# Kernel tuning notes

Hardware: AMD Instinct MI355X
Metric: run time of the kernel (lower is better)

## Reference

```python
import jax, jax.numpy as jnp
import numpy as np

C = 32
C_Z = 128
S = 256
N_SEQ = 256
LN_EPS = 1e-5


def setup_inputs() -> dict:
    key = jax.random.key(0)
    k1, k2, k3, k4 = jax.random.split(key, 4)
    m_si = jax.random.normal(k1, (S, N_SEQ, C), dtype=jnp.float32)
    ln_gamma = jnp.ones((C,), dtype=jnp.float32)
    ln_beta = jnp.zeros((C,), dtype=jnp.float32)
    # nn.Linear(c, 2c, bias=False): weight shape (2c, c)
    W_ab = jax.random.normal(k2, (2 * C, C), dtype=jnp.float32) / np.sqrt(C)
    # nn.Linear(c*c, c_z): weight (c_z, c*c), bias (c_z,)
    W_out = jax.random.normal(k3, (C_Z, C * C), dtype=jnp.float32) / np.sqrt(C * C)
    b_out = jax.random.normal(k4, (C_Z,), dtype=jnp.float32) * 0.01
    return {"m_si": m_si, "ln_gamma": ln_gamma, "ln_beta": ln_beta,
            "W_ab": W_ab, "W_out": W_out, "b_out": b_out}


def reference(m_si, ln_gamma, ln_beta, W_ab, W_out, b_out):
    # LayerNorm over channel dim c
    mu = jnp.mean(m_si, axis=-1, keepdims=True)
    var = jnp.var(m_si, axis=-1, keepdims=True)
    x = (m_si - mu) * jax.lax.rsqrt(var + LN_EPS) * ln_gamma + ln_beta
    # linear_no_bias then chunk into a, b: each (s, n_seq, c)
    ab = jnp.einsum('snc,dc->snd', x, W_ab)
    a, b = ab[..., :C], ab[..., C:]
    # mean over MSA sequences of outer products a[s,i,:] x b[s,j,:]
    # restructured as a contraction over n_seq: (i, j, c, c)
    outer = jnp.einsum('inc,jnd->ijcd', a, b) / N_SEQ
    outer = outer.reshape(S, S, C * C)  # flatten (c, c) -> c*c
    # final linear projection to c_z
    z_ij = jnp.einsum('ijk,zk->ijz', outer, W_out) + b_out
    return z_ij
```

## Files before the change

kernel.cpp:

```cpp
#include <hip/hip_runtime.h>

#define SDIM 256
#define NSEQ 256
#define CDIM 32
#define CZ 128
#define IB 8
#define JB 4

typedef __bf16 bfx8 __attribute__((ext_vector_type(8)));
typedef float fx4 __attribute__((ext_vector_type(4)));
typedef float f32x16 __attribute__((ext_vector_type(16)));
typedef unsigned int u32x4 __attribute__((ext_vector_type(4)));

__device__ __forceinline__ unsigned short f2bf(float f) {
  unsigned int u = __float_as_uint(f);
  u += 0x7fffu + ((u >> 16) & 1u);
  return (unsigned short)(u >> 16);
}

__device__ __forceinline__ unsigned int cvtpk(float lo, float hi) {
  unsigned int r;
  asm("v_cvt_pk_bf16_f32 %0, %1, %2" : "=v"(r) : "v"(lo), "v"(hi));
  return r;
}

__device__ __forceinline__ bfx8 pack8(const fx4 lo, const fx4 hi) {
  bfx8 r;
  r[0] = (__bf16)lo[0]; r[1] = (__bf16)lo[1]; r[2] = (__bf16)lo[2]; r[3] = (__bf16)lo[3];
  r[4] = (__bf16)hi[0]; r[5] = (__bf16)hi[1]; r[6] = (__bf16)hi[2]; r[7] = (__bf16)hi[3];
  return r;
}

__device__ __forceinline__ void gload16(const void* g, void* l) {
  __builtin_amdgcn_global_load_lds((const __attribute__((address_space(1))) unsigned int*)g,
                                   (__attribute__((address_space(3))) unsigned int*)l,
                                   16, 0, 0);
}


__global__ __launch_bounds__(256) void opm_prep(
    const float* __restrict__ m_si, const float* __restrict__ gamma, const float* __restrict__ beta,
    const float* __restrict__ Wab, const float* __restrict__ Wout,
    unsigned short* __restrict__ a_t, unsigned short* __restrict__ b_t,
    unsigned short* __restrict__ w2T)
{
  __shared__ __align__(16) char shbuf[8192];
  const int b = blockIdx.x;
  const int t = threadIdx.x;
  if (b < SDIM) {
    const int s = b;
    const int l = t & 63;
    const int w = t >> 6;
    const int nl = l & 15;
    const int cg = l >> 4;

    bfx8 afr[4];
#pragma unroll
    for (int dt = 0; dt < 4; ++dt) {
      const float* wr = Wab + (dt * 16 + nl) * 32 + cg * 8;
      afr[dt] = pack8(*(const fx4*)wr, *(const fx4*)(wr + 4));
    }
    const fx4 g0 = *(const fx4*)(gamma + cg * 8);
    const fx4 g1 = *(const fx4*)(gamma + cg * 8 + 4);
    const fx4 bt0 = *(const fx4*)(beta + cg * 8);
    const fx4 bt1 = *(const fx4*)(beta + cg * 8 + 4);

#pragma unroll
    for (int p = 0; p < 4; ++p) {
      const int n = p * 64 + w * 16 + nl;
      const float* xr = m_si + (s * 256 + n) * 32 + cg * 8;
      const fx4 v0 = *(const fx4*)xr;
      const fx4 v1 = *(const fx4*)(xr + 4);
      float ps  = v0[0] + v0[1] + v0[2] + v0[3] + v1[0] + v1[1] + v1[2] + v1[3];
      float ps2 = v0[0]*v0[0] + v0[1]*v0[1] + v0[2]*v0[2] + v0[3]*v0[3]
                + v1[0]*v1[0] + v1[1]*v1[1] + v1[2]*v1[2] + v1[3]*v1[3];
      ps  += __shfl_xor(ps, 16);  ps  += __shfl_xor(ps, 32);
      ps2 += __shfl_xor(ps2, 16); ps2 += __shfl_xor(ps2, 32);
      const float mu = ps * 0.03125f;
      const float var = ps2 * 0.03125f - mu * mu;
      const float inv = rsqrtf(var + 1e-5f);
      const fx4 e0 = (v0 - mu) * inv * g0 + bt0;
      const fx4 e1 = (v1 - mu) * inv * g1 + bt1;
      const bfx8 bfr = pack8(e0, e1);

      fx4 dz[4];
#pragma unroll
      for (int dt = 0; dt < 4; ++dt)
        dz[dt] = __builtin_amdgcn_mfma_f32_16x16x32_bf16(afr[dt], bfr, (fx4){0.f,0.f,0.f,0.f}, 0, 0, 0);

#pragma unroll
      for (int dt = 0; dt < 4; ++dt) {
#pragma unroll
        for (int r = 0; r < 4; ++r) {
          const int d = dt * 16 + cg * 4 + r;
          const unsigned short hv = f2bf(dz[dt][r]);
          if (d < 32) a_t[(s * 32 + d) * 256 + n] = hv;
          else        b_t[(s * 32 + (d - 32)) * 256 + n] = hv;
        }
      }
    }
  } else {
    unsigned short* lin = (unsigned short*)shbuf;
    const int blk = b - SDIM;
    const float* wsrc = Wout + blk * 4096;
#pragma unroll
    for (int jj = 0; jj < 4; ++jj) {
      const int q = t + jj * 256;
      const fx4 v = ((const fx4*)wsrc)[q];
      unsigned short* dst = lin + q * 4;
      dst[0] = f2bf(v[0]); dst[1] = f2bf(v[1]); dst[2] = f2bf(v[2]); dst[3] = f2bf(v[3]);
    }
    __syncthreads();
    const int z0 = blk * 4;
#pragma unroll
    for (int w = 0; w < 2; ++w) {
      const int id = t + w * 256;
      const int lz = id & 3;
      const int hh = (id >> 2) & 1;
      const int ks = id >> 3;
      const int z = z0 + lz;
      unsigned short vals[8];
#pragma unroll
      for (int e = 0; e < 8; ++e) {
        const int kp = ks * 16 + hh * 8 + e;
        const int c = (kp & 3) | (((kp >> 8) & 1) << 2) | (((kp >> 2) & 1) << 3) | (((kp >> 9) & 1) << 4);
        const int d = (kp >> 3) & 31;
        vals[e] = lin[lz * 1024 + c * CDIM + d];
      }
      const int dest = ((z >> 5) << 15) + (ks << 9) + (hh << 8) + ((z & 31) << 3);
      *(u32x4*)(w2T + dest) = *(const u32x4*)vals;
    }
  }
}

__global__ __launch_bounds__(512, 4) void opm_main(
    const unsigned short* __restrict__ a_t, const unsigned short* __restrict__ b_t,
    const unsigned short* __restrict__ w2T, const float* __restrict__ bout,
    float* __restrict__ out)
{
  __shared__ __align__(16) char smem[65536];
  char* o_sh = smem;

  const int tid = threadIdx.x;
  const int lane = tid & 63;
  const int wid = tid >> 6;
  const int l31 = lane & 31;
  const int h = lane >> 5;

  const int bxr = blockIdx.x;
  const int xc = bxr & 7;
  const int q8 = bxr >> 3;
  const int it = q8 >> 4;
  const int jt = q8 & 15;
  const int i0 = ((xc & 1) * 16 + it) * IB;
  const int j0 = ((xc >> 1) * 16 + jt) * JB;

  const int wm = wid >> 1;
  const int wn = wid & 1;
  const int wbase = wid * 1024;

  f32x16 acc00 = {}, acc01 = {}, acc10 = {}, acc11 = {};

  auto STAGE = [&](int buf, int nc) {
    const int nbase = nc * 32;
    char* A = smem + 16384 + buf * 16384;
    char* B = smem + 49152 + buf * 8192;
#pragma unroll
    for (int pass = 0; pass < 2; ++pass) {
      const int q = pass * 512 + tid;
      const int row = q >> 2;
      const int gs = (q & 3) ^ ((q >> 3) & 3);
      const unsigned short* src = a_t + ((i0 + (row >> 5)) * 32 + (row & 31)) * 256 + nbase + gs * 8;
      gload16(src, A + pass * 8192 + wbase);
    }
    {
      const int q = tid;
      const int row = q >> 2;
      const int gs = (q & 3) ^ ((q >> 3) & 3);
      const unsigned short* src = b_t + ((j0 + (row >> 5)) * 32 + (row & 31)) * 256 + nbase + gs * 8;
      gload16(src, B + wbase);
    }
  };

  auto COMPUTE = [&](int buf) {
    char* A = smem + 16384 + buf * 16384;
    char* B = smem + 49152 + buf * 8192;
#pragma unroll
    for (int ks = 0; ks < 2; ++ks) {
      const int s = ks * 2 + h;
      bfx8 af0, af1, bf0, bf1;
      { const int r = wm * 64 + l31;      af0 = *(const bfx8*)(A + r * 64 + (((s ^ (r >> 1)) & 3) << 4)); }
      { const int r = wm * 64 + 32 + l31; af1 = *(const bfx8*)(A + r * 64 + (((s ^ (r >> 1)) & 3) << 4)); }
      { const int r = wn * 64 + l31;      bf0 = *(const bfx8*)(B + r * 64 + (((s ^ (r >> 1)) & 3) << 4)); }
      { const int r = wn * 64 + 32 + l31; bf1 = *(const bfx8*)(B + r * 64 + (((s ^ (r >> 1)) & 3) << 4)); }
      __builtin_amdgcn_s_setprio(1);
      acc00 = __builtin_amdgcn_mfma_f32_32x32x16_bf16(af0, bf0, acc00, 0, 0, 0);
      acc01 = __builtin_amdgcn_mfma_f32_32x32x16_bf16(af0, bf1, acc01, 0, 0, 0);
      acc10 = __builtin_amdgcn_mfma_f32_32x32x16_bf16(af1, bf0, acc10, 0, 0, 0);
      acc11 = __builtin_amdgcn_mfma_f32_32x32x16_bf16(af1, bf1, acc11, 0, 0, 0);
      __builtin_amdgcn_s_setprio(0);
    }
  };

  STAGE(0, 0);
#pragma unroll 2
  for (int t = 0; t < 8; ++t) {
    if (t < 7) {
      STAGE((t + 1) & 1, t + 1);
      asm volatile("s_waitcnt vmcnt(3)" ::: "memory");
    } else {
      asm volatile("s_waitcnt vmcnt(0)" ::: "memory");
    }
    __builtin_amdgcn_s_barrier();
    asm volatile("" ::: "memory");
    COMPUTE(t & 1);
    asm volatile("s_waitcnt lgkmcnt(0)" ::: "memory");
    __builtin_amdgcn_s_barrier();
  }

  {
    const f32x16 av[4] = { acc00 * 0.00390625f, acc01 * 0.00390625f,
                           acc10 * 0.00390625f, acc11 * 0.00390625f };
#pragma unroll
    for (int mi = 0; mi < 2; ++mi) {
#pragma unroll
      for (int ni = 0; ni < 2; ++ni) {
        const f32x16 a = av[mi * 2 + ni];
        const int p = (wm * 2 + mi) * 4 + (wn * 2 + ni);
#pragma unroll
        for (int c4 = 0; c4 < 2; ++c4) {
          const int sl = l31 + 32 * h + 64 * c4;
          u32x4 v;
          v[0] = cvtpk(a[8 * c4 + 0], a[8 * c4 + 1]);
          v[1] = cvtpk(a[8 * c4 + 2], a[8 * c4 + 3]);
          v[2] = cvtpk(a[8 * c4 + 4], a[8 * c4 + 5]);
          v[3] = cvtpk(a[8 * c4 + 6], a[8 * c4 + 7]);
          *(u32x4*)(o_sh + p * 2048 + ((sl ^ (p & 7)) << 4)) = v;
        }
      }
    }
  }
  __syncthreads();

  {
    const int ztp = wid & 1;
    const int kh = wid >> 1;
    const unsigned short* wpa = w2T + ((ztp * 2 + 0) << 15) + (h << 8) + (l31 << 3);
    const unsigned short* wpb = w2T + ((ztp * 2 + 1) << 15) + (h << 8) + (l31 << 3);
    const int obase = l31 * 2048;
    const int oxor = l31 & 7;
    const int ks0 = kh * 16;

    bfx8 wa[4], wb[4];
#pragma unroll
    for (int q = 0; q < 4; ++q) {
      wa[q] = *(const bfx8*)(wpa + ((ks0 + q) << 9));
      wb[q] = *(const bfx8*)(wpb + ((ks0 + q) << 9));
    }
    bfx8 oc = *(const bfx8*)(o_sh + obase + ((((ks0 << 1) + h) ^ oxor) << 4));
    bfx8 on = *(const bfx8*)(o_sh + obase + (((((ks0 + 1) << 1) + h) ^ oxor) << 4));

    f32x16 za = {}, zb = {};
#pragma unroll
    for (int st = 0; st < 16; ++st) {
      const int q = st & 3;
      __builtin_amdgcn_s_setprio(1);
      za = __builtin_amdgcn_mfma_f32_32x32x16_bf16(wa[q], oc, za, 0, 0, 0);
      zb = __builtin_amdgcn_mfma_f32_32x32x16_bf16(wb[q], oc, zb, 0, 0, 0);
      __builtin_amdgcn_s_setprio(0);
      oc = on;
      if (st < 14) on = *(const bfx8*)(o_sh + obase + (((((ks0 + st + 2) << 1) + h) ^ oxor) << 4));
      if (st < 12) {
        wa[q] = *(const bfx8*)(wpa + ((ks0 + st + 4) << 9));
        wb[q] = *(const bfx8*)(wpb + ((ks0 + st + 4) << 9));
      }
    }
    __syncthreads();

    const int slot = (kh >> 1) * 2 + ztp;
    auto PWRITE = [&](char* base) {
#pragma unroll
      for (int zs = 0; zs < 2; ++zs) {
        const f32x16& A = zs ? zb : za;
#pragma unroll
        for (int g2 = 0; g2 < 4; ++g2) {
          fx4 v = { A[4 * g2], A[4 * g2 + 1], A[4 * g2 + 2], A[4 * g2 + 3] };
          *(fx4*)(base + zs * 4096 + (((g2 * 2 + h) * 32 + l31) << 4)) = v;
        }
      }
    };
    auto PADD = [&](const char* base) {
#pragma unroll
      for (int zs = 0; zs < 2; ++zs) {
        f32x16& A = zs ? zb : za;
#pragma unroll
        for (int g2 = 0; g2 < 4; ++g2) {
          const fx4 v = *(const fx4*)(base + zs * 4096 + (((g2 * 2 + h) * 32 + l31) << 4));
          A[4 * g2 + 0] += v[0]; A[4 * g2 + 1] += v[1];
          A[4 * g2 + 2] += v[2]; A[4 * g2 + 3] += v[3];
        }
      }
    };
    if (kh & 1) PWRITE(o_sh + slot * 8192);
    __syncthreads();
    if (!(kh & 1)) {
      PADD(o_sh + slot * 8192);
      if (kh == 2) PWRITE(o_sh + 32768 + ztp * 8192);
    }
    __syncthreads();
    if (kh == 0) {
      PADD(o_sh + 32768 + ztp * 8192);
      const int i = i0 + (l31 >> 2), j = j0 + (l31 & 3);
      float* op = out + (i * SDIM + j) * CZ + ztp * 64;
      const float* bp = bout + ztp * 64;
#pragma unroll
      for (int zs = 0; zs < 2; ++zs) {
        const f32x16& A = zs ? zb : za;
#pragma unroll
        for (int g2 = 0; g2 < 4; ++g2) {
          const int zl = zs * 32 + g2 * 8 + h * 4;
          fx4 v = { A[4 * g2], A[4 * g2 + 1], A[4 * g2 + 2], A[4 * g2 + 3] };
          v += *(const fx4*)(bp + zl);
          *(fx4*)(op + zl) = v;
        }
      }
    }
  }
}

extern "C" void kernel_launch(void* const* d_in, const int* in_sizes, int n_in,
                              void* d_out, int out_size, void* d_ws, size_t ws_size,
                              hipStream_t stream) {
  const float* m_si  = (const float*)d_in[0];
  const float* gamma = (const float*)d_in[1];
  const float* beta  = (const float*)d_in[2];
  const float* Wab   = (const float*)d_in[3];
  const float* Wout  = (const float*)d_in[4];
  const float* bout  = (const float*)d_in[5];
  float* out = (float*)d_out;

  char* ws = (char*)d_ws;
  unsigned short* a_t = (unsigned short*)ws;
  unsigned short* b_t = (unsigned short*)(ws + (4u << 20));
  unsigned short* w2T = (unsigned short*)(ws + (8u << 20));

  opm_prep<<<dim3(SDIM + 32), dim3(256), 0, stream>>>(m_si, gamma, beta, Wab, Wout, a_t, b_t, w2T);
  opm_main<<<dim3(2048), dim3(512), 0, stream>>>(a_t, b_t, w2T, bout, out);
}
```

Measured before the change: 77.93 us.

## Triple-buffer LDS staging with prefetch depth two and split A/B loads

Moves the main loop from double to triple buffering in LDS so global loads run two chunks ahead, raising shared memory to 72KB. The A-tile load is issued at the start of each iteration and the B-tile load after the first k-half, with an extra barrier between the two halves. The aim is to hide global-load latency behind the MFMA work. In exchange it adds a barrier per iteration and uses more LDS per block, which could affect residency.

```diff
diff --git a/kernel.cpp b/kernel.cpp
--- a/kernel.cpp
+++ b/kernel.cpp
@@ -138,7 +138,7 @@
     const unsigned short* __restrict__ w2T, const float* __restrict__ bout,
     float* __restrict__ out)
 {
-  __shared__ __align__(16) char smem[65536];
+  __shared__ __align__(16) char smem[73728];
   char* o_sh = smem;
 
   const int tid = threadIdx.x;
@@ -161,10 +161,9 @@
 
   f32x16 acc00 = {}, acc01 = {}, acc10 = {}, acc11 = {};
 
-  auto STAGE = [&](int buf, int nc) {
+  auto STAGE_A = [&](int buf, int nc) {
     const int nbase = nc * 32;
-    char* A = smem + 16384 + buf * 16384;
-    char* B = smem + 49152 + buf * 8192;
+    char* A = smem + buf * 16384;
 #pragma unroll
     for (int pass = 0; pass < 2; ++pass) {
       const int q = pass * 512 + tid;
@@ -173,50 +172,56 @@
       const unsigned short* src = a_t + ((i0 + (row >> 5)) * 32 + (row & 31)) * 256 + nbase + gs * 8;
       gload16(src, A + pass * 8192 + wbase);
     }
-    {
-      const int q = tid;
-      const int row = q >> 2;
-      const int gs = (q & 3) ^ ((q >> 3) & 3);
-      const unsigned short* src = b_t + ((j0 + (row >> 5)) * 32 + (row & 31)) * 256 + nbase + gs * 8;
-      gload16(src, B + wbase);
-    }
   };
-
-  auto COMPUTE = [&](int buf) {
-    char* A = smem + 16384 + buf * 16384;
+  auto STAGE_B = [&](int buf, int nc) {
+    const int nbase = nc * 32;
     char* B = smem + 49152 + buf * 8192;
-#pragma unroll
-    for (int ks = 0; ks < 2; ++ks) {
-      const int s = ks * 2 + h;
-      bfx8 af0, af1, bf0, bf1;
-      { const int r = wm * 64 + l31;      af0 = *(const bfx8*)(A + r * 64 + (((s ^ (r >> 1)) & 3) << 4)); }
-      { const int r = wm * 64 + 32 + l31; af1 = *(const bfx8*)(A + r * 64 + (((s ^ (r >> 1)) & 3) << 4)); }
-      { const int r = wn * 64 + l31;      bf0 = *(const bfx8*)(B + r * 64 + (((s ^ (r >> 1)) & 3) << 4)); }
-      { const int r = wn * 64 + 32 + l31; bf1 = *(const bfx8*)(B + r * 64 + (((s ^ (r >> 1)) & 3) << 4)); }
-      __builtin_amdgcn_s_setprio(1);
-      acc00 = __builtin_amdgcn_mfma_f32_32x32x16_bf16(af0, bf0, acc00, 0, 0, 0);
-      acc01 = __builtin_amdgcn_mfma_f32_32x32x16_bf16(af0, bf1, acc01, 0, 0, 0);
-      acc10 = __builtin_amdgcn_mfma_f32_32x32x16_bf16(af1, bf0, acc10, 0, 0, 0);
-      acc11 = __builtin_amdgcn_mfma_f32_32x32x16_bf16(af1, bf1, acc11, 0, 0, 0);
-      __builtin_amdgcn_s_setprio(0);
-    }
+    const int q = tid;
+    const int row = q >> 2;
+    const int gs = (q & 3) ^ ((q >> 3) & 3);
+    const unsigned short* src = b_t + ((j0 + (row >> 5)) * 32 + (row & 31)) * 256 + nbase + gs * 8;
+    gload16(src, B + wbase);
   };
 
-  STAGE(0, 0);
-#pragma unroll 2
-  for (int t = 0; t < 8; ++t) {
-    if (t < 7) {
-      STAGE((t + 1) & 1, t + 1);
-      asm volatile("s_waitcnt vmcnt(3)" ::: "memory");
-    } else {
-      asm volatile("s_waitcnt vmcnt(0)" ::: "memory");
-    }
+  auto HALF = [&](int buf, int ks) {
+    char* A = smem + buf * 16384;
+    char* B = smem + 49152 + buf * 8192;
+    const int s = ks * 2 + h;
+    bfx8 af0, af1, bf0, bf1;
+    { const int r = wm * 64 + l31;      af0 = *(const bfx8*)(A + r * 64 + (((s ^ (r >> 1)) & 3) << 4)); }
+    { const int r = wm * 64 + 32 + l31; af1 = *(const bfx8*)(A + r * 64 + (((s ^ (r >> 1)) & 3) << 4)); }
+    { const int r = wn * 64 + l31;      bf0 = *(const bfx8*)(B + r * 64 + (((s ^ (r >> 1)) & 3) << 4)); }
+    { const int r = wn * 64 + 32 + l31; bf1 = *(const bfx8*)(B + r * 64 + (((s ^ (r >> 1)) & 3) << 4)); }
+    __builtin_amdgcn_s_setprio(1);
+    acc00 = __builtin_amdgcn_mfma_f32_32x32x16_bf16(af0, bf0, acc00, 0, 0, 0);
+    acc01 = __builtin_amdgcn_mfma_f32_32x32x16_bf16(af0, bf1, acc01, 0, 0, 0);
+    acc10 = __builtin_amdgcn_mfma_f32_32x32x16_bf16(af1, bf0, acc10, 0, 0, 0);
+    acc11 = __builtin_amdgcn_mfma_f32_32x32x16_bf16(af1, bf1, acc11, 0, 0, 0);
+    __builtin_amdgcn_s_setprio(0);
+  };
+
+  STAGE_A(0, 0); STAGE_B(0, 0);
+  STAGE_A(1, 1); STAGE_B(1, 1);
+
+#pragma unroll
+  for (int c = 0; c < 8; ++c) {
+    const int buf = c % 3;
+    if (c + 2 < 8) STAGE_A((c + 2) % 3, c + 2);
+    if (c <= 5)      { asm volatile("s_waitcnt vmcnt(5)" ::: "memory"); }
+    else if (c == 6) { asm volatile("s_waitcnt vmcnt(3)" ::: "memory"); }
+    else             { asm volatile("s_waitcnt vmcnt(0)" ::: "memory"); }
     __builtin_amdgcn_s_barrier();
     asm volatile("" ::: "memory");
-    COMPUTE(t & 1);
+    HALF(buf, 0);
+    asm volatile("s_waitcnt lgkmcnt(0)" ::: "memory");
+    __builtin_amdgcn_s_barrier();
+    if (c + 2 < 8) STAGE_B((c + 2) % 3, c + 2);
+    asm volatile("" ::: "memory");
+    HALF(buf, 1);
     asm volatile("s_waitcnt lgkmcnt(0)" ::: "memory");
     __builtin_amdgcn_s_barrier();
   }
+  __syncthreads();
 
   {
     const f32x16 av[4] = { acc00 * 0.00390625f, acc01 * 0.00390625f,
```

New measurement: 74.99 us. 3.8% less time.
